# Kernel optimization log

Measured on AMD Instinct MI355X. Metric: run time of the kernel, lower is better.

## Reference

```python
import jax, jax.numpy as jnp
import numpy as np

DIM = 1024
NUM_HEADS = 16
HEAD_DIM = DIM // NUM_HEADS
ROPE_BASE = 10000.0


def _rope_cos_sin(seq_len, head_dim, dtype):
    # inv_freq over even indices of head_dim
    inv_freq = 1.0 / (ROPE_BASE ** (jnp.arange(0, head_dim, 2, dtype=jnp.float32) / head_dim))
    t = jnp.arange(seq_len, dtype=jnp.float32)
    freqs = jnp.einsum('i,j->ij', t, inv_freq)        # [N, D/2]
    emb = jnp.concatenate([freqs, freqs], axis=-1)    # [N, D]
    return jnp.cos(emb).astype(dtype), jnp.sin(emb).astype(dtype)


def _rotate_half(x):
    x1, x2 = jnp.split(x, 2, axis=-1)
    return jnp.concatenate([-x2, x1], axis=-1)


def setup_inputs() -> dict:
    key = jax.random.key(0)
    k1, k2, k3 = jax.random.split(key, 3)
    B, N = 2, 2048
    x = jax.random.normal(k1, (B, N, DIM), dtype=jnp.float32)
    # torch Linear weights: [out_features, in_features]; init scale ~1/sqrt(dim)
    Wqkv = jax.random.normal(k2, (3 * DIM, DIM), dtype=jnp.float32) * (DIM ** -0.5)
    Wproj = jax.random.normal(k3, (DIM, DIM), dtype=jnp.float32) * (DIM ** -0.5)
    return {"x": x, "Wqkv": Wqkv, "Wproj": Wproj}


def reference(x, Wqkv, Wproj):
    B, N, C = x.shape
    H, D = NUM_HEADS, HEAD_DIM
    # QKV projection: [B,N,3C] -> [3,B,H,N,D]
    qkv = jnp.einsum('bnc,oc->bno', x, Wqkv)
    qkv = qkv.reshape(B, N, 3, H, D).transpose(2, 0, 3, 1, 4)
    q, k, v = qkv[0], qkv[1], qkv[2]                  # each [B,H,N,D]
    # RoPE
    cos, sin = _rope_cos_sin(N, D, x.dtype)           # [N,D] each
    cos = cos[None, None, :, :]
    sin = sin[None, None, :, :]
    q = q * cos + _rotate_half(q) * sin
    k = k * cos + _rotate_half(k) * sin
    # scaled dot-product attention (non-causal, no mask, no dropout)
    scale = 1.0 / jnp.sqrt(jnp.asarray(D, dtype=x.dtype))
    scores = jnp.einsum('bhnd,bhmd->bhnm', q, k) * scale
    attn = jax.nn.softmax(scores, axis=-1)
    out = jnp.einsum('bhnm,bhmd->bhnd', attn, v)      # [B,H,N,D]
    out = out.transpose(0, 2, 1, 3).reshape(B, N, C)
    return jnp.einsum('bnc,oc->bno', out, Wproj)
```

## Files before the change

kernel.cpp:

```cpp
#include <hip/hip_runtime.h>
#include <hip/hip_bf16.h>

#define SEQ   2048
#define DIMC  1024
#define NH    16
#define HD    64
#define QKV3  3072
#define NB    2
#define SCALE_LOG2E 0.18033688011112042f

typedef __attribute__((ext_vector_type(8)))  short bf16x8;
typedef __attribute__((ext_vector_type(4)))  float f32x4;
typedef __attribute__((ext_vector_type(16))) float f32x16;

__device__ __forceinline__ unsigned short f2bf(float f){
  union { float f; unsigned int u; } v; v.f = f;
  return (unsigned short)((v.u + 0x7fffu + ((v.u >> 16) & 1u)) >> 16);
}
__device__ __forceinline__ float bf2f(unsigned short h){
  union { unsigned int u; float f; } v; v.u = ((unsigned int)h) << 16; return v.f;
}
__device__ __forceinline__ int packbf2(float a, float b){
  __hip_bfloat162 h = __float22bfloat162_rn(make_float2(a, b));
  int r; __builtin_memcpy(&r, &h, 4); return r;
}
__device__ __forceinline__ void async_lds16(void* lds, const void* g){
  __builtin_amdgcn_global_load_lds(
      (const __attribute__((address_space(1))) void*)g,
      (__attribute__((address_space(3))) void*)lds, 16, 0, 0);
}

__global__ __launch_bounds__(256) void k_prep(const float* __restrict__ x,
                                              const float* __restrict__ wqkv,
                                              const float* __restrict__ wproj,
                                              unsigned short* __restrict__ xb,
                                              unsigned short* __restrict__ wqkvb,
                                              unsigned short* __restrict__ wprojb,
                                              float2* __restrict__ tab){
  const int b = blockIdx.x, tid = threadIdx.x;
  if (b < 8192){
    const float* in; unsigned short* out; int i;
    if (b < 4096)      { in = x;     out = xb;     i = b * 256 + tid; }
    else if (b < 7168) { in = wqkv;  out = wqkvb;  i = (b - 4096) * 256 + tid; }
    else               { in = wproj; out = wprojb; i = (b - 7168) * 256 + tid; }
    const float4 v = ((const float4*)in)[i];
    union { unsigned short s[4]; unsigned long long u; } p;
    p.s[0] = f2bf(v.x); p.s[1] = f2bf(v.y); p.s[2] = f2bf(v.z); p.s[3] = f2bf(v.w);
    *(unsigned long long*)(out + (size_t)i * 4) = p.u;
  } else {
    const int idx = (b - 8192) * 256 + tid;
    const int n = idx >> 5, j = idx & 31;
    const float inv = 1.0f / powf(10000.0f, (float)(2 * j) * (1.0f / 64.0f));
    const float f = (float)n * inv;
    tab[idx] = make_float2(cosf(f), sinf(f));
  }
}

template<int OUT_BF16>
__global__ __launch_bounds__(256) void k_gemm(const unsigned short* __restrict__ A,
                                              const unsigned short* __restrict__ Bm,
                                              void* __restrict__ Cp, int M, int N, int K){
  __shared__ unsigned short As[128 * 64];
  __shared__ unsigned short Bs[128 * 64];
  const int tid = threadIdx.x, wave = tid >> 6, lane = tid & 63;
  const int nbn = N >> 7;
  const int bm = blockIdx.x / nbn, bn = blockIdx.x % nbn;
  const int m0 = bm << 7, n0 = bn << 7;
  const int wr = wave >> 1, wc = wave & 1;

  f32x4 acc[4][4];
#pragma unroll
  for (int i = 0; i < 4; i++)
#pragma unroll
    for (int j = 0; j < 4; j++) acc[i][j] = (f32x4){0.f, 0.f, 0.f, 0.f};

  for (int k0 = 0; k0 < K; k0 += 64){
#pragma unroll
    for (int c = 0; c < 4; c++){
      const int e = c * 2048 + tid * 8;
      const int row = e >> 6, col = e & 63;
      async_lds16(As + c * 2048 + wave * 512, A + (size_t)(m0 + row) * K + k0 + col);
      async_lds16(Bs + c * 2048 + wave * 512, Bm + (size_t)(n0 + row) * K + k0 + col);
    }
    __syncthreads();
#pragma unroll
    for (int ks = 0; ks < 2; ks++){
      const int kk = ks * 32 + (lane >> 4) * 8;
      bf16x8 af[4], bfr[4];
#pragma unroll
      for (int i = 0; i < 4; i++){
        af[i]  = *(const bf16x8*)&As[(wr * 64 + i * 16 + (lane & 15)) * 64 + kk];
        bfr[i] = *(const bf16x8*)&Bs[(wc * 64 + i * 16 + (lane & 15)) * 64 + kk];
      }
#pragma unroll
      for (int i = 0; i < 4; i++)
#pragma unroll
        for (int j = 0; j < 4; j++)
          acc[i][j] = __builtin_amdgcn_mfma_f32_16x16x32_bf16(af[i], bfr[j], acc[i][j], 0, 0, 0);
    }
    __syncthreads();
  }
#pragma unroll
  for (int i = 0; i < 4; i++)
#pragma unroll
    for (int j = 0; j < 4; j++)
#pragma unroll
      for (int r = 0; r < 4; r++){
        const int row = m0 + wr * 64 + i * 16 + (lane >> 4) * 4 + r;
        const int col = n0 + wc * 64 + j * 16 + (lane & 15);
        const float v = acc[i][j][r];
        if constexpr (OUT_BF16) ((unsigned short*)Cp)[(size_t)row * N + col] = f2bf(v);
        else                    ((float*)Cp)[(size_t)row * N + col] = v;
      }
}

__global__ __launch_bounds__(256) void k_rope(const unsigned short* __restrict__ qkv,
                                              const float2* __restrict__ tab,
                                              unsigned short* __restrict__ Qb,
                                              unsigned short* __restrict__ Kswz){
  unsigned int idx = blockIdx.x * 256 + threadIdx.x;
  const int j = idx & 3; idx >>= 2;
  const int n = idx & 2047; idx >>= 11;
  const int h = idx & 15; idx >>= 4;
  const int b = idx & 1;
  const int which = idx >> 1;
  const size_t rowbase = ((size_t)(b * SEQ + n)) * QKV3 + which * DIMC + h * HD;
  const bf16x8 lo = *(const bf16x8*)&qkv[rowbase + j * 8];
  const bf16x8 hi = *(const bf16x8*)&qkv[rowbase + 32 + j * 8];
  union { unsigned short s[8]; bf16x8 v; } olo, ohi;
#pragma unroll
  for (int t = 0; t < 8; t++){
    const float2 cs = tab[n * 32 + j * 8 + t];
    const float xl = bf2f((unsigned short)lo[t]), xh = bf2f((unsigned short)hi[t]);
    float yl = xl * cs.x - xh * cs.y;
    float yh = xh * cs.x + xl * cs.y;
    if (which == 0){ yl *= SCALE_LOG2E; yh *= SCALE_LOG2E; }
    olo.s[t] = f2bf(yl); ohi.s[t] = f2bf(yh);
  }
  const size_t orow = (((size_t)(b * NH + h)) * SEQ + n) * HD;
  if (which == 0){
    *(bf16x8*)&Qb[orow + j * 8]      = olo.v;
    *(bf16x8*)&Qb[orow + 32 + j * 8] = ohi.v;
  } else {
    const int s = (n & 7) << 3;
    *(bf16x8*)&Kswz[orow + ((j * 8) ^ s)]      = olo.v;
    *(bf16x8*)&Kswz[orow + ((32 + j * 8) ^ s)] = ohi.v;
  }
}

__global__ __launch_bounds__(256) void k_vt(const unsigned short* __restrict__ qkv,
                                            unsigned short* __restrict__ Vt){
  __shared__ unsigned short t[64 * 72];
  const int tid = threadIdx.x;
  const int nt = blockIdx.x & 31, h = (blockIdx.x >> 5) & 15, b = blockIdx.x >> 9;
  const int n0 = nt * 64;
#pragma unroll
  for (int p = 0; p < 2; p++){
    const int e = p * 2048 + tid * 8;
    const int r = e >> 6, c = e & 63;
    *(bf16x8*)&t[r * 72 + c] =
        *(const bf16x8*)&qkv[((size_t)(b * SEQ + n0 + r)) * QKV3 + 2048 + h * 64 + c];
  }
  __syncthreads();
#pragma unroll
  for (int p = 0; p < 2; p++){
    const int e = p * 2048 + tid * 8;
    const int d = e >> 6, nn = e & 63;
    const int sw = (d & 7) << 3;
    union { unsigned short s[8]; bf16x8 v; } o;
#pragma unroll
    for (int q = 0; q < 8; q++) o.s[q] = t[((nn ^ sw) + q) * 72 + d];
    *(bf16x8*)&Vt[(((size_t)(b * NH + h)) * HD + d) * SEQ + n0 + nn] = o.v;
  }
}

__global__ __launch_bounds__(256) void k_attn(const unsigned short* __restrict__ Q,
                                              const unsigned short* __restrict__ Kg,
                                              const unsigned short* __restrict__ Vg,
                                              unsigned short* __restrict__ AO){
  __shared__ unsigned short Ks[2][64 * 64];
  __shared__ unsigned short Vs[2][64 * 64];
  const int tid = threadIdx.x, wave = tid >> 6, lane = tid & 63;
  const int bh = blockIdx.x & 31, qt = blockIdx.x >> 5;
  const size_t base = (size_t)bh * (SEQ * HD);
  const int q32 = lane & 31, hi = lane >> 5, hi8 = hi << 3;
  const int sw = (q32 & 7) << 3;
  const int q0w = qt * 128 + wave * 32;

  bf16x8 qf[4];
#pragma unroll
  for (int kc = 0; kc < 4; kc++)
    qf[kc] = *(const bf16x8*)&Q[base + (size_t)(q0w + q32) * HD + kc * 16 + hi8];

  f32x16 oacc[2];
#pragma unroll
  for (int md = 0; md < 2; md++)
#pragma unroll
    for (int r = 0; r < 16; r++) oacc[md][r] = 0.f;
  float mrow = -INFINITY, lrow = 0.f;

  const int srow = lane >> 3, scol = (lane & 7) * 8;

#pragma unroll
  for (int i = 0; i < 2; i++){
    const int c = wave * 2 + i, row = c * 8 + srow;
    async_lds16(&Ks[0][c * 512], &Kg[base + (size_t)row * HD + scol]);
    async_lds16(&Vs[0][c * 512], &Vg[base + (size_t)row * SEQ + scol]);
  }
  asm volatile("s_waitcnt vmcnt(0)" ::: "memory");
  __syncthreads();

#pragma unroll 1
  for (int t = 0; t < 32; t++){
    const int cur = t & 1;
    if (t < 31){
      const int kv0 = (t + 1) * 64;
#pragma unroll
      for (int i = 0; i < 2; i++){
        const int c = wave * 2 + i, row = c * 8 + srow;
        async_lds16(&Ks[cur ^ 1][c * 512], &Kg[base + (size_t)(kv0 + row) * HD + scol]);
        async_lds16(&Vs[cur ^ 1][c * 512], &Vg[base + (size_t)row * SEQ + kv0 + scol]);
      }
    }

    f32x16 s0, s1;
#pragma unroll
    for (int r = 0; r < 16; r++){ s0[r] = 0.f; s1[r] = 0.f; }
    __builtin_amdgcn_s_setprio(1);
#pragma unroll
    for (int kc = 0; kc < 4; kc++){
      const int col = (kc * 16 + hi8) ^ sw;
      const bf16x8 k0 = *(const bf16x8*)&Ks[cur][q32 * 64 + col];
      const bf16x8 k1 = *(const bf16x8*)&Ks[cur][(32 + q32) * 64 + col];
      s0 = __builtin_amdgcn_mfma_f32_32x32x16_bf16(k0, qf[kc], s0, 0, 0, 0);
      s1 = __builtin_amdgcn_mfma_f32_32x32x16_bf16(k1, qf[kc], s1, 0, 0, 0);
    }
    __builtin_amdgcn_s_setprio(0);

    float m8[8];
#pragma unroll
    for (int r = 0; r < 8; r++)
      m8[r] = fmaxf(fmaxf(s0[r], s0[r + 8]), fmaxf(s1[r], s1[r + 8]));
    float mx = fmaxf(fmaxf(fmaxf(m8[0], m8[4]), fmaxf(m8[1], m8[5])),
                     fmaxf(fmaxf(m8[2], m8[6]), fmaxf(m8[3], m8[7])));
    mx = fmaxf(mx, __shfl_xor(mx, 32));
    if (!__all(mx <= mrow)){
      const float mnew = fmaxf(mrow, mx);
      const float alpha = __builtin_amdgcn_exp2f(mrow - mnew);
      mrow = mnew;
      lrow *= alpha;
#pragma unroll
      for (int md = 0; md < 2; md++)
#pragma unroll
        for (int r = 0; r < 16; r++) oacc[md][r] *= alpha;
    }
#pragma unroll
    for (int r = 0; r < 16; r++){
      s0[r] = __builtin_amdgcn_exp2f(s0[r] - mrow);
      s1[r] = __builtin_amdgcn_exp2f(s1[r] - mrow);
    }
    float a8[8];
#pragma unroll
    for (int r = 0; r < 8; r++)
      a8[r] = (s0[r] + s0[r + 8]) + (s1[r] + s1[r + 8]);
    float rs = ((a8[0] + a8[1]) + (a8[2] + a8[3])) + ((a8[4] + a8[5]) + (a8[6] + a8[7]));
    rs += __shfl_xor(rs, 32);
    lrow += rs;

#pragma unroll
    for (int g2 = 0; g2 < 4; g2++){
      float pj[8];
#pragma unroll
      for (int t2 = 0; t2 < 8; t2++) pj[t2] = (g2 < 2) ? s0[(g2 & 1) * 8 + t2] : s1[(g2 & 1) * 8 + t2];
      const int X0 = packbf2(pj[0], pj[1]), X1 = packbf2(pj[2], pj[3]);
      const int Y0 = packbf2(pj[4], pj[5]), Y1 = packbf2(pj[6], pj[7]);
      const int pX0 = __shfl_xor(X0, 32), pX1 = __shfl_xor(X1, 32);
      const int pY0 = __shfl_xor(Y0, 32), pY1 = __shfl_xor(Y1, 32);
      union { int w[4]; bf16x8 v; } pb;
      pb.w[0] = hi ? pY0 : X0;
      pb.w[1] = hi ? pY1 : X1;
      pb.w[2] = hi ? Y0 : pX0;
      pb.w[3] = hi ? Y1 : pX1;
      __builtin_amdgcn_s_setprio(1);
#pragma unroll
      for (int md = 0; md < 2; md++){
        const bf16x8 av = *(const bf16x8*)&Vs[cur][(md * 32 + q32) * 64 + ((g2 * 16 + hi8) ^ sw)];
        oacc[md] = __builtin_amdgcn_mfma_f32_32x32x16_bf16(av, pb.v, oacc[md], 0, 0, 0);
      }
      __builtin_amdgcn_s_setprio(0);
    }

    asm volatile("s_waitcnt vmcnt(0)" ::: "memory");
    __syncthreads();
  }

  const float rl = 1.0f / lrow;
  const int b = bh >> 4, h = bh & 15;
  const size_t obase = ((size_t)(b * SEQ + q0w + q32)) * DIMC + h * HD;
#pragma unroll
  for (int md = 0; md < 2; md++)
#pragma unroll
    for (int a = 0; a < 4; a++){
      const int d0 = md * 32 + a * 8 + hi * 4;
      int2 wv;
      wv.x = packbf2(oacc[md][a * 4 + 0] * rl, oacc[md][a * 4 + 1] * rl);
      wv.y = packbf2(oacc[md][a * 4 + 2] * rl, oacc[md][a * 4 + 3] * rl);
      *(int2*)&AO[obase + d0] = wv;
    }
}

extern "C" void kernel_launch(void* const* d_in, const int* in_sizes, int n_in,
                              void* d_out, int out_size, void* d_ws, size_t ws_size,
                              hipStream_t stream){
  const float* x     = (const float*)d_in[0];
  const float* Wqkv  = (const float*)d_in[1];
  const float* Wproj = (const float*)d_in[2];
  float* out = (float*)d_out;
  char* ws = (char*)d_ws;

  unsigned short* xb     = (unsigned short*)(ws);
  unsigned short* wqkvb  = (unsigned short*)(ws +  8388608);
  unsigned short* wprojb = (unsigned short*)(ws + 14680064);
  unsigned short* qkvb   = (unsigned short*)(ws + 16777216);
  float2*         tab    = (float2*)        (ws + 41943040);
  unsigned short* Qb     = (unsigned short*)(ws + 42467328);
  unsigned short* Kb     = (unsigned short*)(ws + 50855936);
  unsigned short* Vtb    = (unsigned short*)(ws + 59244544);
  unsigned short* AOb    = (unsigned short*)(ws);

  k_prep<<<8448, 256, 0, stream>>>(x, Wqkv, Wproj, xb, wqkvb, wprojb, tab);
  k_gemm<1><<<32 * 24, 256, 0, stream>>>(xb, wqkvb, (void*)qkvb, 4096, 3072, 1024);
  k_rope<<<2048, 256, 0, stream>>>(qkvb, tab, Qb, Kb);
  k_vt<<<1024, 256, 0, stream>>>(qkvb, Vtb);
  k_attn<<<512, 256, 0, stream>>>(Qb, Kb, Vtb, AOb);
  k_gemm<0><<<32 * 8, 256, 0, stream>>>(AOb, wprojb, (void*)out, 4096, 1024, 1024);
}
```

Baseline: 238.5 us.

## Use 128-wide KV tiles in attention, permute K rows, fuse rope and V transpose

The attention kernel now stages 128 keys per iteration instead of 64, halving the number of loop iterations, barriers and online-softmax rescale checks. K rows are written in a permuted order so the score accumulator layout feeds the PV MFMA directly, which removes the cross-lane shuffles used to build the P operand. The rope and V-transpose kernels are merged into one launch. In exchange, LDS use doubles to 64 KB per block and register pressure rises, which may lower occupancy.

```diff
diff --git a/kernel.cpp b/kernel.cpp
--- a/kernel.cpp
+++ b/kernel.cpp
@@ -114,63 +114,65 @@
       }
 }
 
-__global__ __launch_bounds__(256) void k_rope(const unsigned short* __restrict__ qkv,
+__global__ __launch_bounds__(256) void k_post(const unsigned short* __restrict__ qkv,
                                               const float2* __restrict__ tab,
                                               unsigned short* __restrict__ Qb,
-                                              unsigned short* __restrict__ Kswz){
-  unsigned int idx = blockIdx.x * 256 + threadIdx.x;
-  const int j = idx & 3; idx >>= 2;
-  const int n = idx & 2047; idx >>= 11;
-  const int h = idx & 15; idx >>= 4;
-  const int b = idx & 1;
-  const int which = idx >> 1;
-  const size_t rowbase = ((size_t)(b * SEQ + n)) * QKV3 + which * DIMC + h * HD;
-  const bf16x8 lo = *(const bf16x8*)&qkv[rowbase + j * 8];
-  const bf16x8 hi = *(const bf16x8*)&qkv[rowbase + 32 + j * 8];
-  union { unsigned short s[8]; bf16x8 v; } olo, ohi;
-#pragma unroll
-  for (int t = 0; t < 8; t++){
-    const float2 cs = tab[n * 32 + j * 8 + t];
-    const float xl = bf2f((unsigned short)lo[t]), xh = bf2f((unsigned short)hi[t]);
-    float yl = xl * cs.x - xh * cs.y;
-    float yh = xh * cs.x + xl * cs.y;
-    if (which == 0){ yl *= SCALE_LOG2E; yh *= SCALE_LOG2E; }
-    olo.s[t] = f2bf(yl); ohi.s[t] = f2bf(yh);
-  }
-  const size_t orow = (((size_t)(b * NH + h)) * SEQ + n) * HD;
-  if (which == 0){
-    *(bf16x8*)&Qb[orow + j * 8]      = olo.v;
-    *(bf16x8*)&Qb[orow + 32 + j * 8] = ohi.v;
+                                              unsigned short* __restrict__ Kswz,
+                                              unsigned short* __restrict__ Vt){
+  __shared__ unsigned short t[64 * 72];
+  if (blockIdx.x < 2048){
+    unsigned int idx = blockIdx.x * 256 + threadIdx.x;
+    const int j = idx & 3; idx >>= 2;
+    const int n = idx & 2047; idx >>= 11;
+    const int h = idx & 15; idx >>= 4;
+    const int b = idx & 1;
+    const int which = idx >> 1;
+    const size_t rowbase = ((size_t)(b * SEQ + n)) * QKV3 + which * DIMC + h * HD;
+    const bf16x8 lo = *(const bf16x8*)&qkv[rowbase + j * 8];
+    const bf16x8 hi = *(const bf16x8*)&qkv[rowbase + 32 + j * 8];
+    union { unsigned short s[8]; bf16x8 v; } olo, ohi;
+#pragma unroll
+    for (int u = 0; u < 8; u++){
+      const float2 cs = tab[n * 32 + j * 8 + u];
+      const float xl = bf2f((unsigned short)lo[u]), xh = bf2f((unsigned short)hi[u]);
+      float yl = xl * cs.x - xh * cs.y;
+      float yh = xh * cs.x + xl * cs.y;
+      if (which == 0){ yl *= SCALE_LOG2E; yh *= SCALE_LOG2E; }
+      olo.s[u] = f2bf(yl); ohi.s[u] = f2bf(yh);
+    }
+    if (which == 0){
+      const size_t orow = (((size_t)(b * NH + h)) * SEQ + n) * HD;
+      *(bf16x8*)&Qb[orow + j * 8]      = olo.v;
+      *(bf16x8*)&Qb[orow + 32 + j * 8] = ohi.v;
+    } else {
+      const int np = (n & ~31) | (n & 0x13) | ((n & 4) << 1) | ((n & 8) >> 1);
+      const int s = (np & 7) << 3;
+      const size_t orow = (((size_t)(b * NH + h)) * SEQ + np) * HD;
+      *(bf16x8*)&Kswz[orow + ((j * 8) ^ s)]      = olo.v;
+      *(bf16x8*)&Kswz[orow + ((32 + j * 8) ^ s)] = ohi.v;
+    }
   } else {
-    const int s = (n & 7) << 3;
-    *(bf16x8*)&Kswz[orow + ((j * 8) ^ s)]      = olo.v;
-    *(bf16x8*)&Kswz[orow + ((32 + j * 8) ^ s)] = ohi.v;
-  }
-}
-
-__global__ __launch_bounds__(256) void k_vt(const unsigned short* __restrict__ qkv,
-                                            unsigned short* __restrict__ Vt){
-  __shared__ unsigned short t[64 * 72];
-  const int tid = threadIdx.x;
-  const int nt = blockIdx.x & 31, h = (blockIdx.x >> 5) & 15, b = blockIdx.x >> 9;
-  const int n0 = nt * 64;
-#pragma unroll
-  for (int p = 0; p < 2; p++){
-    const int e = p * 2048 + tid * 8;
-    const int r = e >> 6, c = e & 63;
-    *(bf16x8*)&t[r * 72 + c] =
-        *(const bf16x8*)&qkv[((size_t)(b * SEQ + n0 + r)) * QKV3 + 2048 + h * 64 + c];
-  }
-  __syncthreads();
-#pragma unroll
-  for (int p = 0; p < 2; p++){
-    const int e = p * 2048 + tid * 8;
-    const int d = e >> 6, nn = e & 63;
-    const int sw = (d & 7) << 3;
-    union { unsigned short s[8]; bf16x8 v; } o;
-#pragma unroll
-    for (int q = 0; q < 8; q++) o.s[q] = t[((nn ^ sw) + q) * 72 + d];
-    *(bf16x8*)&Vt[(((size_t)(b * NH + h)) * HD + d) * SEQ + n0 + nn] = o.v;
+    const int i2 = blockIdx.x - 2048, tid = threadIdx.x;
+    const int nt = i2 & 31, h = (i2 >> 5) & 15, b = i2 >> 9;
+    const int n0 = nt * 64;
+#pragma unroll
+    for (int p = 0; p < 2; p++){
+      const int e = p * 2048 + tid * 8;
+      const int r = e >> 6, c = e & 63;
+      *(bf16x8*)&t[r * 72 + c] =
+          *(const bf16x8*)&qkv[((size_t)(b * SEQ + n0 + r)) * QKV3 + 2048 + h * 64 + c];
+    }
+    __syncthreads();
+#pragma unroll
+    for (int p = 0; p < 2; p++){
+      const int e = p * 2048 + tid * 8;
+      const int d = e >> 6, nn = e & 63;
+      const int sw = (d & 7) << 3;
+      union { unsigned short s[8]; bf16x8 v; } o;
+#pragma unroll
+      for (int q = 0; q < 8; q++) o.s[q] = t[((nn ^ sw) + q) * 72 + d];
+      *(bf16x8*)&Vt[(((size_t)(b * NH + h)) * HD + d) * SEQ + n0 + nn] = o.v;
+    }
   }
 }
 
@@ -178,8 +180,8 @@
                                               const unsigned short* __restrict__ Kg,
                                               const unsigned short* __restrict__ Vg,
                                               unsigned short* __restrict__ AO){
-  __shared__ unsigned short Ks[2][64 * 64];
-  __shared__ unsigned short Vs[2][64 * 64];
+  __shared__ unsigned short Ks[2][128 * 64];
+  __shared__ unsigned short Vs[2][64 * 128];
   const int tid = threadIdx.x, wave = tid >> 6, lane = tid & 63;
   const int bh = blockIdx.x & 31, qt = blockIdx.x >> 5;
   const size_t base = (size_t)bh * (SEQ * HD);
@@ -199,50 +201,52 @@
     for (int r = 0; r < 16; r++) oacc[md][r] = 0.f;
   float mrow = -INFINITY, lrow = 0.f;
 
-  const int srow = lane >> 3, scol = (lane & 7) * 8;
-
-#pragma unroll
-  for (int i = 0; i < 2; i++){
-    const int c = wave * 2 + i, row = c * 8 + srow;
-    async_lds16(&Ks[0][c * 512], &Kg[base + (size_t)row * HD + scol]);
-    async_lds16(&Vs[0][c * 512], &Vg[base + (size_t)row * SEQ + scol]);
-  }
+  const int krow = wave * 8 + (lane >> 3), kcol = (lane & 7) * 8;
+  const int vd   = wave * 4 + (lane >> 4), vcol = (lane & 15) * 8;
+
+  auto stage = [&](int buf, int kv0){
+#pragma unroll
+    for (int r = 0; r < 4; r++)
+      async_lds16(&Ks[buf][r * 2048 + wave * 512],
+                  &Kg[base + (size_t)(kv0 + r * 32 + krow) * HD + kcol]);
+#pragma unroll
+    for (int r = 0; r < 4; r++)
+      async_lds16(&Vs[buf][r * 2048 + wave * 512],
+                  &Vg[base + (size_t)(r * 16 + vd) * SEQ + kv0 + vcol]);
+  };
+
+  stage(0, 0);
   asm volatile("s_waitcnt vmcnt(0)" ::: "memory");
   __syncthreads();
 
 #pragma unroll 1
-  for (int t = 0; t < 32; t++){
+  for (int t = 0; t < 16; t++){
     const int cur = t & 1;
-    if (t < 31){
-      const int kv0 = (t + 1) * 64;
-#pragma unroll
-      for (int i = 0; i < 2; i++){
-        const int c = wave * 2 + i, row = c * 8 + srow;
-        async_lds16(&Ks[cur ^ 1][c * 512], &Kg[base + (size_t)(kv0 + row) * HD + scol]);
-        async_lds16(&Vs[cur ^ 1][c * 512], &Vg[base + (size_t)row * SEQ + kv0 + scol]);
+    if (t < 15) stage(cur ^ 1, (t + 1) * 128);
+
+    f32x16 s[4];
+#pragma unroll
+    for (int k2 = 0; k2 < 4; k2++)
+#pragma unroll
+      for (int r = 0; r < 16; r++) s[k2][r] = 0.f;
+    __builtin_amdgcn_s_setprio(1);
+#pragma unroll
+    for (int k2 = 0; k2 < 4; k2++)
+#pragma unroll
+      for (int kc = 0; kc < 4; kc++){
+        const bf16x8 kf = *(const bf16x8*)&Ks[cur][(k2 * 32 + q32) * 64 + ((kc * 16 + hi8) ^ sw)];
+        s[k2] = __builtin_amdgcn_mfma_f32_32x32x16_bf16(kf, qf[kc], s[k2], 0, 0, 0);
       }
-    }
-
-    f32x16 s0, s1;
-#pragma unroll
-    for (int r = 0; r < 16; r++){ s0[r] = 0.f; s1[r] = 0.f; }
-    __builtin_amdgcn_s_setprio(1);
-#pragma unroll
-    for (int kc = 0; kc < 4; kc++){
-      const int col = (kc * 16 + hi8) ^ sw;
-      const bf16x8 k0 = *(const bf16x8*)&Ks[cur][q32 * 64 + col];
-      const bf16x8 k1 = *(const bf16x8*)&Ks[cur][(32 + q32) * 64 + col];
-      s0 = __builtin_amdgcn_mfma_f32_32x32x16_bf16(k0, qf[kc], s0, 0, 0, 0);
-      s1 = __builtin_amdgcn_mfma_f32_32x32x16_bf16(k1, qf[kc], s1, 0, 0, 0);
-    }
     __builtin_amdgcn_s_setprio(0);
 
-    float m8[8];
-#pragma unroll
-    for (int r = 0; r < 8; r++)
-      m8[r] = fmaxf(fmaxf(s0[r], s0[r + 8]), fmaxf(s1[r], s1[r + 8]));
-    float mx = fmaxf(fmaxf(fmaxf(m8[0], m8[4]), fmaxf(m8[1], m8[5])),
-                     fmaxf(fmaxf(m8[2], m8[6]), fmaxf(m8[3], m8[7])));
+    float m16[16];
+#pragma unroll
+    for (int r = 0; r < 16; r++)
+      m16[r] = fmaxf(fmaxf(s[0][r], s[1][r]), fmaxf(s[2][r], s[3][r]));
+#pragma unroll
+    for (int r = 0; r < 8; r++) m16[r] = fmaxf(m16[r], m16[r + 8]);
+    float mx = fmaxf(fmaxf(fmaxf(m16[0], m16[4]), fmaxf(m16[1], m16[5])),
+                     fmaxf(fmaxf(m16[2], m16[6]), fmaxf(m16[3], m16[7])));
     mx = fmaxf(mx, __shfl_xor(mx, 32));
     if (!__all(mx <= mrow)){
       const float mnew = fmaxf(mrow, mx);
@@ -255,40 +259,38 @@
         for (int r = 0; r < 16; r++) oacc[md][r] *= alpha;
     }
 #pragma unroll
-    for (int r = 0; r < 16; r++){
-      s0[r] = __builtin_amdgcn_exp2f(s0[r] - mrow);
-      s1[r] = __builtin_amdgcn_exp2f(s1[r] - mrow);
-    }
-    float a8[8];
-#pragma unroll
-    for (int r = 0; r < 8; r++)
-      a8[r] = (s0[r] + s0[r + 8]) + (s1[r] + s1[r + 8]);
-    float rs = ((a8[0] + a8[1]) + (a8[2] + a8[3])) + ((a8[4] + a8[5]) + (a8[6] + a8[7]));
+    for (int k2 = 0; k2 < 4; k2++)
+#pragma unroll
+      for (int r = 0; r < 16; r++)
+        s[k2][r] = __builtin_amdgcn_exp2f(s[k2][r] - mrow);
+    float a16[16];
+#pragma unroll
+    for (int r = 0; r < 16; r++)
+      a16[r] = (s[0][r] + s[1][r]) + (s[2][r] + s[3][r]);
+#pragma unroll
+    for (int r = 0; r < 8; r++) a16[r] += a16[r + 8];
+    float rs = ((a16[0] + a16[1]) + (a16[2] + a16[3])) + ((a16[4] + a16[5]) + (a16[6] + a16[7]));
     rs += __shfl_xor(rs, 32);
     lrow += rs;
 
-#pragma unroll
-    for (int g2 = 0; g2 < 4; g2++){
-      float pj[8];
-#pragma unroll
-      for (int t2 = 0; t2 < 8; t2++) pj[t2] = (g2 < 2) ? s0[(g2 & 1) * 8 + t2] : s1[(g2 & 1) * 8 + t2];
-      const int X0 = packbf2(pj[0], pj[1]), X1 = packbf2(pj[2], pj[3]);
-      const int Y0 = packbf2(pj[4], pj[5]), Y1 = packbf2(pj[6], pj[7]);
-      const int pX0 = __shfl_xor(X0, 32), pX1 = __shfl_xor(X1, 32);
-      const int pY0 = __shfl_xor(Y0, 32), pY1 = __shfl_xor(Y1, 32);
+    __builtin_amdgcn_s_setprio(1);
+#pragma unroll
+    for (int g2 = 0; g2 < 8; g2++){
+      const int k2 = g2 >> 1, off = (g2 & 1) * 8;
       union { int w[4]; bf16x8 v; } pb;
-      pb.w[0] = hi ? pY0 : X0;
-      pb.w[1] = hi ? pY1 : X1;
-      pb.w[2] = hi ? Y0 : pX0;
-      pb.w[3] = hi ? Y1 : pX1;
-      __builtin_amdgcn_s_setprio(1);
+      pb.w[0] = packbf2(s[k2][off + 0], s[k2][off + 1]);
+      pb.w[1] = packbf2(s[k2][off + 2], s[k2][off + 3]);
+      pb.w[2] = packbf2(s[k2][off + 4], s[k2][off + 5]);
+      pb.w[3] = packbf2(s[k2][off + 6], s[k2][off + 7]);
+      const int col = g2 * 16 + hi8;
+      const int colA = ((col & 63) ^ sw) | (col & 64);
 #pragma unroll
       for (int md = 0; md < 2; md++){
-        const bf16x8 av = *(const bf16x8*)&Vs[cur][(md * 32 + q32) * 64 + ((g2 * 16 + hi8) ^ sw)];
+        const bf16x8 av = *(const bf16x8*)&Vs[cur][(md * 32 + q32) * 128 + colA];
         oacc[md] = __builtin_amdgcn_mfma_f32_32x32x16_bf16(av, pb.v, oacc[md], 0, 0, 0);
       }
-      __builtin_amdgcn_s_setprio(0);
-    }
+    }
+    __builtin_amdgcn_s_setprio(0);
 
     asm volatile("s_waitcnt vmcnt(0)" ::: "memory");
     __syncthreads();
@@ -330,8 +332,7 @@
 
   k_prep<<<8448, 256, 0, stream>>>(x, Wqkv, Wproj, xb, wqkvb, wprojb, tab);
   k_gemm<1><<<32 * 24, 256, 0, stream>>>(xb, wqkvb, (void*)qkvb, 4096, 3072, 1024);
-  k_rope<<<2048, 256, 0, stream>>>(qkvb, tab, Qb, Kb);
-  k_vt<<<1024, 256, 0, stream>>>(qkvb, Vtb);
+  k_post<<<3072, 256, 0, stream>>>(qkvb, tab, Qb, Kb, Vtb);
   k_attn<<<512, 256, 0, stream>>>(Qb, Kb, Vtb, AOb);
   k_gemm<0><<<32 * 8, 256, 0, stream>>>(AOb, wprojb, (void*)out, 4096, 1024, 1024);
 }
```

Result: faster. 221.3 us (-7.2%).
